# Performance work log

Measured on AMD Instinct MI355X. Metric: run time of the kernel, lower is better.

## Reference

```python
import jax, jax.numpy as jnp
import numpy as np

B, S, D, F, E, K, R, H = 4, 1024, 1024, 512, 8, 2, 64, 256
TEMP = 1.0          # step=0 -> 0.5+0.5*cos(0)=1.0, clamp(min=0.1) -> 1.0
BW, EW, ZW = 0.3, 0.1, 1e-4


def fq(t):
    """Per-tensor symmetric int8 fake-quant with straight-through estimator."""
    s = jnp.maximum(jnp.max(jnp.abs(t)) / 127.0, 1e-8)
    q = jnp.clip(jnp.round(t / s), -128, 127) * s
    return t + jax.lax.stop_gradient(q - t)


def lora_lin(h, W, A, Bm):
    # base weight is frozen (requires_grad=False) and fake-quantized
    y = h @ fq(jax.lax.stop_gradient(W)).T + (h @ Bm.T) @ A.T
    return fq(y)


def ffn(h, w1, a1, b1, w2, a2, b2, w3, a3, b3):
    # use_swiglu=True path: gate = sigmoid(w3(x)); out = w2(w1(x)*gate); dropout=eval identity
    gate = jax.nn.sigmoid(lora_lin(h, w3, a3, b3))
    out = lora_lin(lora_lin(h, w1, a1, b1) * gate, w2, a2, b2)
    return fq(out)


def setup_inputs() -> dict:
    key = jax.random.key(0)
    k = jax.random.split(key, 32)
    n = lambda i, shp: jax.random.normal(k[i], shp, dtype=jnp.float32) * 0.02
    return {
        "x": jax.random.normal(k[0], (B, S, D), dtype=jnp.float32),
        "scorer_w": n(1, (E, D)), "scorer_b": jnp.zeros((E,), jnp.float32),
        "p1_w": n(2, (H, D)), "p1_b": jnp.zeros((H,), jnp.float32),
        "p2_w": n(3, (E, H)), "p2_b": jnp.zeros((E,), jnp.float32),
        "ew1_w": n(4, (E, F, D)), "ew1_a": n(5, (E, F, R)), "ew1_b": n(6, (E, R, D)),
        "ew2_w": n(7, (E, D, F)), "ew2_a": n(8, (E, D, R)), "ew2_b": n(9, (E, R, F)),
        "ew3_w": n(10, (E, F, D)), "ew3_a": n(11, (E, F, R)), "ew3_b": n(12, (E, R, D)),
        "s1_w": n(13, (F, D)), "s1_a": n(14, (F, R)), "s1_b": n(15, (R, D)),
        "s2_w": n(16, (D, F)), "s2_a": n(17, (D, R)), "s2_b": n(18, (R, F)),
        "s3_w": n(19, (F, D)), "s3_a": n(20, (F, R)), "s3_b": n(21, (R, D)),
    }


def reference(x, scorer_w, scorer_b, p1_w, p1_b, p2_w, p2_b,
              ew1_w, ew1_a, ew1_b, ew2_w, ew2_a, ew2_b, ew3_w, ew3_a, ew3_b,
              s1_w, s1_a, s1_b, s2_w, s2_a, s2_b, s3_w, s3_a, s3_b):
    xf = x.reshape(-1, D)                                           # [T, D]
    # --- router (per-token) ---
    base = (xf @ scorer_w.T + scorer_b) / TEMP                      # [T, E]
    policy = jax.nn.softmax(jax.nn.relu(xf @ p1_w.T + p1_b) @ p2_w.T + p2_b, axis=-1)
    scores = jax.nn.softmax((base + policy) * 0.5, axis=-1)         # fp32 softmax
    entropy = -(scores * jnp.log(scores + 1e-6)).sum(-1).mean()
    z_loss = ZW * (jax.nn.logsumexp(base, axis=-1) ** 2).mean()
    weights, indices = jax.lax.top_k(scores, K)                     # [T, K]
    weights = weights * TEMP
    cw = (jax.nn.one_hot(indices, E, dtype=weights.dtype) * weights[..., None]).sum(1)  # [T, E]
    usage = cw.sum(0)                                               # [E]
    uf = usage / (usage.mean() + 1e-6)
    balance_loss = BW * jnp.var(uf, ddof=1) - EW * entropy + z_loss
    # --- expert dispatch: dense masked combine (faithful to weighted scatter-add) ---
    eout = jax.vmap(lambda w1, a1, b1, w2, a2, b2, w3, a3, b3:
                    ffn(xf, w1, a1, b1, w2, a2, b2, w3, a3, b3))(
        ew1_w, ew1_a, ew1_b, ew2_w, ew2_a, ew2_b, ew3_w, ew3_a, ew3_b)  # [E, T, D]
    y = jnp.einsum('te,etd->td', cw, eout)                          # weighted combine
    z = ffn(xf, s1_w, s1_a, s1_b, s2_w, s2_a, s2_b, s3_w, s3_a, s3_b)
    out = (y + z).reshape(x.shape)
    return (out, usage, balance_loss, jnp.float32(0.0), jnp.float32(0.0))
```

## Files before the change

kernel.cpp:

```cpp
#include <hip/hip_runtime.h>

#define TTOK 4096
#define DDIM 1024
#define FDIM 512
#define NEXP 8
#define HDIM 256
#define RLORA 64
#define CROWS 14336

using u16 = unsigned short;
using f4v = __attribute__((ext_vector_type(4))) float;
using bfrag = __attribute__((ext_vector_type(8))) short;
using u16x8 = __attribute__((ext_vector_type(8))) unsigned short;

static __device__ __forceinline__ float bf2f(u16 u) {
  union { unsigned int u; float f; } x; x.u = ((unsigned int)u) << 16; return x.f;
}
static __device__ __forceinline__ u16 f2bf(float f) {
  union { float f; unsigned int u; } x; x.f = f;
  unsigned int r = (x.u + 0x7fffu + ((x.u >> 16) & 1u)) >> 16;
  return (u16)r;
}
static __device__ __forceinline__ float fq1(float t, float s) {
  float q = rintf(t / s);
  q = fminf(fmaxf(q, -128.f), 127.f);
  return q * s;
}

struct GemmGArgs {
  const u16* A; const u16* B; u16* C;
  const int* tokmap; const int2* blkmap; const int* nbrow;
};

#define STAGE1(d, kt, h, l) \
  __builtin_amdgcn_global_load_lds( \
    (const __attribute__((address_space(1))) void*)(gs[(h)*2+(l)] + (size_t)(kt)*64), \
    (__attribute__((address_space(3))) void*)&lds[(d)*32768 + (h)*8192 + (tid + (l)*512)*8], \
    16, 0, 0)

template <int MODE>
__global__ __launch_bounds__(512, 2) void gemm256g(GemmGArgs g) {
  const int bid = blockIdx.x;
  const int logical = (bid & 7) * 28 + (bid >> 3);
  const int br = logical >> 2;
  if (br >= g.nbrow[0]) return;
  const int2 bm = g.blkmap[br];
  const int e = bm.x;
  const int m0 = bm.y;
  const int n0 = (logical & 3) * 256;
  const int tid = threadIdx.x;
  const int lane = tid & 63;
  const int wave = tid >> 6;
  const int wr = wave >> 2;
  const int wc = wave & 3;

  constexpr int K = MODE ? 1024 : 512;
  const u16* Bp = g.B + (size_t)e * (MODE ? 1048576 : 524288);

  __shared__ u16 lds[65536];

  const u16* gs[8];
#pragma unroll
  for (int h = 0; h < 4; h++)
#pragma unroll
    for (int l = 0; l < 2; l++) {
      const int slot = tid + l * 512;
      const int row = slot >> 3, p = slot & 7;
      const int glog = p ^ (row & 7);
      const u16* basep;
      if (h < 2) {
        const int grow = m0 + h * 128 + row;
        const int t = MODE ? g.tokmap[grow] : grow;
        basep = g.A + (size_t)t * K;
      } else {
        basep = Bp + (size_t)(n0 + (h - 2) * 128 + row) * K;
      }
      gs[h * 2 + l] = basep + glog * 8;
    }

  f4v acc[8][4];
#pragma unroll
  for (int i = 0; i < 8; i++)
#pragma unroll
    for (int j = 0; j < 4; j++) acc[i][j] = (f4v){0.f, 0.f, 0.f, 0.f};

  const int q = lane >> 4;
  const int lx = lane & 7;
  const int l15 = lane & 15;

#pragma unroll
  for (int h = 0; h < 4; h++) { STAGE1(0, 0, h, 0); STAGE1(0, 0, h, 1); }
  __syncthreads();

  constexpr int nt = K >> 6;
  for (int kt = 0; kt < nt; ++kt) {
    const int d = kt & 1;
    const int dn = d ^ 1;
    const bool more = (kt + 1 < nt);
#pragma unroll
    for (int kk = 0; kk < 2; ++kk) {
      if (more) {
        if (kk == 0) { STAGE1(dn, kt + 1, 0, 0); STAGE1(dn, kt + 1, 0, 1);
                       STAGE1(dn, kt + 1, 1, 0); STAGE1(dn, kt + 1, 1, 1); }
        else         { STAGE1(dn, kt + 1, 2, 0); STAGE1(dn, kt + 1, 2, 1);
                       STAGE1(dn, kt + 1, 3, 0); STAGE1(dn, kt + 1, 3, 1); }
      }
      bfrag afr[8], bfr[4];
      const int pa = ((kk * 4 + q) ^ lx) << 3;
      const int abase = d * 32768 + wr * 8192 + l15 * 64 + pa;
#pragma unroll
      for (int mi = 0; mi < 8; mi++) afr[mi] = *(const bfrag*)&lds[abase + mi * 1024];
      const int bbase = d * 32768 + (2 + (wc >> 1)) * 8192 + (((wc & 1) << 6) + l15) * 64 + pa;
#pragma unroll
      for (int ni = 0; ni < 4; ni++) bfr[ni] = *(const bfrag*)&lds[bbase + ni * 1024];
      __builtin_amdgcn_s_setprio(1);
#pragma unroll
      for (int mi = 0; mi < 8; mi++)
#pragma unroll
        for (int ni = 0; ni < 4; ni++)
          acc[mi][ni] = __builtin_amdgcn_mfma_f32_16x16x32_bf16(afr[mi], bfr[ni], acc[mi][ni], 0, 0, 0);
      __builtin_amdgcn_s_setprio(0);
    }
    __syncthreads();
  }

  const int crow0 = m0 + wr * 128 + q * 4;

  if (MODE == 1) {
    u16* stage = lds;
    const int lrow0 = wr * 128 + q * 4;
    if (wc >= 2) {
      const int lc = (wc - 2) * 64 + l15;
#pragma unroll
      for (int mi = 0; mi < 8; mi++)
#pragma unroll
        for (int ni = 0; ni < 4; ni++)
#pragma unroll
          for (int r = 0; r < 4; r++)
            stage[(lrow0 + mi * 16 + r) * 136 + lc + ni * 16] = f2bf(acc[mi][ni][r]);
    }
    __syncthreads();
    if (wc < 2) {
      const int lc = wc * 64 + l15;
      const int fbase = (n0 >> 1) + lc;
#pragma unroll
      for (int mi = 0; mi < 8; mi++)
#pragma unroll
        for (int r = 0; r < 4; r++) {
          const int rowg = crow0 + mi * 16 + r;
          const int lr = lrow0 + mi * 16 + r;
#pragma unroll
          for (int ni = 0; ni < 4; ni++) {
            float y1 = acc[mi][ni][r];
            float y3 = bf2f(stage[lr * 136 + lc + ni * 16]);
            float h = y1 / (1.f + __expf(-y3));
            g.C[(size_t)rowg * FDIM + fbase + ni * 16] = f2bf(h);
          }
        }
    }
  } else {
    const int ccol0 = n0 + wc * 64 + l15;
#pragma unroll
    for (int mi = 0; mi < 8; mi++)
#pragma unroll
      for (int ni = 0; ni < 4; ni++) {
        const int col = ccol0 + ni * 16;
#pragma unroll
        for (int r = 0; r < 4; r++)
          g.C[(size_t)(crow0 + mi * 16 + r) * 1024 + col] = f2bf(acc[mi][ni][r]);
      }
  }
}

struct MidArgs {
  const u16* A64; const u16* B64; u16* C64; const float* bias64;
  const u16* A0; const u16* B0;
  const u16* Wb;
  u16* C13; u16* C2e;
  const float* amaxP;
};

__global__ __launch_bounds__(256) void mid_kernel(MidArgs g) {
  __shared__ u16 smem[25600];
  __shared__ float s_sw;
  const int bid = blockIdx.x;
  const int tid = threadIdx.x;
  const int lane = tid & 63;
  const int wave = tid >> 6;

  if (bid < 256) {
    const int wr = wave >> 1, wc = wave & 1;
    const int m0 = (bid & 63) * 64, n0 = (bid >> 6) * 64;
    const int K = DDIM, N = HDIM;
    u16* As = smem;
    u16* Bs = smem + 2048;

    const int ldrow = tid >> 2;
    const int swzcol = (((tid & 3) ^ ((tid >> 3) & 3)) << 3);
    const u16* ga = g.A64 + (size_t)(m0 + ldrow) * K + swzcol;
    const u16* gb = g.B64 + (size_t)(n0 + ldrow) * K + swzcol;

    f4v acc[2][2];
#pragma unroll
    for (int i = 0; i < 2; i++)
#pragma unroll
      for (int j = 0; j < 2; j++) acc[i][j] = (f4v){0.f, 0.f, 0.f, 0.f};

    const int rbase = lane & 15;
    const int q = lane >> 4;
    const int pg = (q ^ ((rbase >> 1) & 3)) << 3;
    const int arow = (wr << 5) + rbase;
    const int brow = (wc << 5) + rbase;

    for (int kt = 0; kt < K; kt += 32) {
      __builtin_amdgcn_global_load_lds((const __attribute__((address_space(1))) void*)(ga),
          (__attribute__((address_space(3))) void*)&As[tid * 8], 16, 0, 0);
      __builtin_amdgcn_global_load_lds((const __attribute__((address_space(1))) void*)(gb),
          (__attribute__((address_space(3))) void*)&Bs[tid * 8], 16, 0, 0);
      ga += 32; gb += 32;
      __syncthreads();
      bfrag af[2], bf[2];
#pragma unroll
      for (int mi = 0; mi < 2; mi++)
        af[mi] = *(const bfrag*)&As[(arow + mi * 16) * 32 + pg];
#pragma unroll
      for (int ni = 0; ni < 2; ni++)
        bf[ni] = *(const bfrag*)&Bs[(brow + ni * 16) * 32 + pg];
#pragma unroll
      for (int mi = 0; mi < 2; mi++)
#pragma unroll
        for (int ni = 0; ni < 2; ni++)
          acc[mi][ni] = __builtin_amdgcn_mfma_f32_16x16x32_bf16(af[mi], bf[ni], acc[mi][ni], 0, 0, 0);
      __syncthreads();
    }

    const int crow0 = m0 + (wr << 5) + ((lane >> 4) << 2);
    const int ccol0 = n0 + (wc << 5) + (lane & 15);
#pragma unroll
    for (int mi = 0; mi < 2; mi++)
#pragma unroll
      for (int ni = 0; ni < 2; ni++) {
        const int n = ccol0 + ni * 16;
        const float b = g.bias64[n];
#pragma unroll
        for (int r = 0; r < 4; r++) {
          float v = fmaxf(acc[mi][ni][r] + b, 0.f);
          g.C64[(size_t)(crow0 + mi * 16 + r) * N + n] = f2bf(v);
        }
      }
    return;
  }

  const int fid = bid - 256;
  const int z = fid >> 6;
  const int rem = fid & 63;
  const int bx = rem & 7, by = rem >> 3;
  const bool is13 = z < 18;
  if (is13 ? (bx >= 4) : (by >= 4)) return;
  const int N = is13 ? 1024 : 512;
  const int K = 64;
  const u16* Ap = is13 ? g.A0 + (size_t)z * 32768 : g.A0 + 589824 + (size_t)(z - 18) * 65536;
  const u16* Bp = is13 ? g.B0 + (size_t)z * 65536 : g.B0 + 1179648 + (size_t)(z - 18) * 32768;
  const u16* Wf = g.Wb + (size_t)z * 524288;
  u16* Cb; int flag;
  if (is13) {
    const int slot = (z >= 16) ? 8 : (z & 7);
    Cb = g.C13 + (size_t)slot * 1048576;
    flag = (z >= 8 && z < 16) || z == 17 ? 2 : 1;
  } else {
    Cb = g.C2e + (size_t)(z - 18) * 524288;
    flag = 0;
  }

  const int wr = wave >> 1, wc = wave & 1;
  const int m0 = bx * 128, n0 = by * 128;
  u16* As = smem;
  u16* Bs = smem + 4096;
  u16* stage = smem + 8192;

  if (wave == 0) {
    float m = fmaxf(g.amaxP[z * 128 + lane], g.amaxP[z * 128 + 64 + lane]);
#pragma unroll
    for (int off = 32; off > 0; off >>= 1) m = fmaxf(m, __shfl_xor(m, off));
    if (lane == 0) s_sw = fmaxf(m / 127.f, 1e-8f);
  }

  const int ldrow = tid >> 2;
  const int swzcol = (((tid & 3) ^ ((tid >> 3) & 3)) << 3);
  const u16* ga = Ap + (size_t)(m0 + ldrow) * K + swzcol;
  const u16* gb = Bp + (size_t)(n0 + ldrow) * K + swzcol;
  const size_t rowstep = (size_t)64 * K;

  f4v acc[4][4];
#pragma unroll
  for (int i = 0; i < 4; i++)
#pragma unroll
    for (int j = 0; j < 4; j++) acc[i][j] = (f4v){0.f, 0.f, 0.f, 0.f};

  const int rbase = lane & 15;
  const int q = lane >> 4;
  const int pg = (q ^ ((rbase >> 1) & 3)) << 3;
  const int arow = (wr << 6) + rbase;
  const int brow = (wc << 6) + rbase;

  for (int kt = 0; kt < K; kt += 32) {
    __builtin_amdgcn_global_load_lds((const __attribute__((address_space(1))) void*)(ga),
        (__attribute__((address_space(3))) void*)&As[tid * 8], 16, 0, 0);
    __builtin_amdgcn_global_load_lds((const __attribute__((address_space(1))) void*)(ga + rowstep),
        (__attribute__((address_space(3))) void*)&As[(256 + tid) * 8], 16, 0, 0);
    __builtin_amdgcn_global_load_lds((const __attribute__((address_space(1))) void*)(gb),
        (__attribute__((address_space(3))) void*)&Bs[tid * 8], 16, 0, 0);
    __builtin_amdgcn_global_load_lds((const __attribute__((address_space(1))) void*)(gb + rowstep),
        (__attribute__((address_space(3))) void*)&Bs[(256 + tid) * 8], 16, 0, 0);
    ga += 32; gb += 32;
    __syncthreads();
    bfrag af[4], bf[4];
#pragma unroll
    for (int mi = 0; mi < 4; mi++)
      af[mi] = *(const bfrag*)&As[(arow + mi * 16) * 32 + pg];
#pragma unroll
    for (int ni = 0; ni < 4; ni++)
      bf[ni] = *(const bfrag*)&Bs[(brow + ni * 16) * 32 + pg];
#pragma unroll
    for (int mi = 0; mi < 4; mi++)
#pragma unroll
      for (int ni = 0; ni < 4; ni++)
        acc[mi][ni] = __builtin_amdgcn_mfma_f32_16x16x32_bf16(af[mi], bf[ni], acc[mi][ni], 0, 0, 0);
    __syncthreads();
  }

  const int lrow0 = (wr << 6) + ((lane >> 4) << 2);
  const int lcol0 = (wc << 6) + (lane & 15);
#pragma unroll
  for (int mi = 0; mi < 4; mi++)
#pragma unroll
    for (int ni = 0; ni < 4; ni++) {
      const int n = lcol0 + ni * 16;
#pragma unroll
      for (int r = 0; r < 4; r++)
        stage[(lrow0 + mi * 16 + r) * 136 + n] = f2bf(acc[mi][ni][r]);
    }
  __syncthreads();
  const float sw = s_sw;

  const int dm0 = flag ? (((m0 >> 7) << 8) + (flag == 2 ? 128 : 0)) : m0;
#pragma unroll
  for (int j = 0; j < 8; j++) {
    const int s = j * 256 + tid;
    const int lr = s >> 4;
    const int n8 = (s & 15) << 3;
    const u16x8 wv = *(const u16x8*)&Wf[(size_t)(m0 + lr) * N + n0 + n8];
    const bfrag sv = *(const bfrag*)&stage[lr * 136 + n8];
    u16x8 o;
#pragma unroll
    for (int k = 0; k < 8; k++)
      o[k] = f2bf(fq1(bf2f(wv[k]), sw) + bf2f((u16)sv[k]));
    *(u16x8*)&Cb[(size_t)(dm0 + lr) * N + n0 + n8] = o;
  }
}

struct PrepArgs {
  const float* W[27]; u16* Wraw; float* amaxP;
  const float* xf; u16* xfb;
  const float* p1w; u16* p1wb;
  const float* Asrc[27]; u16* Adst;
  const float* Bsrc[27]; u16* Bdst;
};
__global__ __launch_bounds__(256) void prep_kernel(PrepArgs a) {
  const int bid = blockIdx.x;
  const int tid = threadIdx.x;
  if (bid < 3456) {
    const int t = bid >> 7;
    const int bx = bid & 127;
    const float4* src = (const float4*)a.W[t];
    ushort4* dst = (ushort4*)(a.Wraw + (size_t)t * 524288);
    const int i0 = bx * 256 + tid;
    float4 v0 = src[i0];
    float4 v1 = src[i0 + 32768];
    float4 v2 = src[i0 + 65536];
    float4 v3 = src[i0 + 98304];
    ushort4 o0, o1, o2, o3;
    o0.x = f2bf(v0.x); o0.y = f2bf(v0.y); o0.z = f2bf(v0.z); o0.w = f2bf(v0.w);
    o1.x = f2bf(v1.x); o1.y = f2bf(v1.y); o1.z = f2bf(v1.z); o1.w = f2bf(v1.w);
    o2.x = f2bf(v2.x); o2.y = f2bf(v2.y); o2.z = f2bf(v2.z); o2.w = f2bf(v2.w);
    o3.x = f2bf(v3.x); o3.y = f2bf(v3.y); o3.z = f2bf(v3.z); o3.w = f2bf(v3.w);
    dst[i0] = o0; dst[i0 + 32768] = o1; dst[i0 + 65536] = o2; dst[i0 + 98304] = o3;
    float m01 = fmaxf(fmaxf(fabsf(v0.x), fabsf(v0.y)), fmaxf(fabsf(v0.z), fabsf(v0.w)));
    float m11 = fmaxf(fmaxf(fabsf(v1.x), fabsf(v1.y)), fmaxf(fabsf(v1.z), fabsf(v1.w)));
    float m21 = fmaxf(fmaxf(fabsf(v2.x), fabsf(v2.y)), fmaxf(fabsf(v2.z), fabsf(v2.w)));
    float m31 = fmaxf(fmaxf(fabsf(v3.x), fabsf(v3.y)), fmaxf(fabsf(v3.z), fabsf(v3.w)));
    float lmax = fmaxf(fmaxf(m01, m11), fmaxf(m21, m31));
#pragma unroll
    for (int off = 32; off > 0; off >>= 1) lmax = fmaxf(lmax, __shfl_xor(lmax, off));
    __shared__ float wm[4];
    if ((tid & 63) == 0) wm[tid >> 6] = lmax;
    __syncthreads();
    if (tid == 0)
      a.amaxP[t * 128 + bx] = fmaxf(fmaxf(wm[0], wm[1]), fmaxf(wm[2], wm[3]));
    return;
  }
  const int cid = bid - 3456;
  const int slice = cid >> 10;
  const int g0 = (cid & 1023) * 256 + tid;
  const int stride = 262144;
  if (slice == 0) {
    for (int i = g0; i < 1048576; i += stride) {
      float4 v = ((const float4*)a.xf)[i];
      ushort4 o; o.x = f2bf(v.x); o.y = f2bf(v.y); o.z = f2bf(v.z); o.w = f2bf(v.w);
      ((ushort4*)a.xfb)[i] = o;
    }
  } else if (slice == 1) {
    for (int i = g0; i < 65536; i += stride) {
      float4 v = ((const float4*)a.p1w)[i];
      ushort4 o; o.x = f2bf(v.x); o.y = f2bf(v.y); o.z = f2bf(v.z); o.w = f2bf(v.w);
      ((ushort4*)a.p1wb)[i] = o;
    }
  } else if (slice == 2) {
    for (int i = g0; i < 1179648; i += stride) {
      int t, off;
      if (i < 589824) { t = i >> 15; off = i & 32767; }
      else { int j = i - 589824; t = 18 + (j >> 16); off = j & 65535; }
      a.Adst[i] = f2bf(a.Asrc[t][off]);
    }
  } else {
    for (int i = g0; i < 1474560; i += stride) {
      int t, src;
      if (i < 1179648) { t = i >> 16; int off = i & 65535; src = (off & 63) * 1024 + (off >> 6); }
      else { int j = i - 1179648; t = 18 + (j >> 15); int off = j & 32767; src = (off & 63) * 512 + (off >> 6); }
      a.Bdst[i] = f2bf(a.Bsrc[t][src]);
    }
  }
}

struct RouterArgs {
  const float* xf; const u16* ph;
  const float* sw; const float* sb;
  const float* p2w; const float* p2b;
  int* idx2; float2* wb;
  float* partials;
  int* histArr;
};
__global__ __launch_bounds__(256) void router_kernel(RouterArgs a) {
  __shared__ float sw[8][1024];
  __shared__ float p2[8][256];
  __shared__ float blog[16][8];
  __shared__ float plog[16][8];
  __shared__ int hist[8];
  const int tid = threadIdx.x;
  {
    const float4* s0 = (const float4*)a.sw;
    float4* d0 = (float4*)&sw[0][0];
    for (int i = tid; i < 2048; i += 256) d0[i] = s0[i];
    const float4* s1 = (const float4*)a.p2w;
    float4* d1 = (float4*)&p2[0][0];
    for (int i = tid; i < 512; i += 256) d1[i] = s1[i];
  }
  if (tid < 8) hist[tid] = 0;
  __syncthreads();
  const int tl = tid >> 4, s = tid & 15;
  const int token = blockIdx.x * 16 + tl;
  {
    float acc[8] = {0,0,0,0,0,0,0,0}, pacc[8] = {0,0,0,0,0,0,0,0};
    const float4* xrow = (const float4*)(a.xf + (size_t)token * 1024);
    for (int i = 0; i < 16; i++) {
      const int d4 = i * 16 + s;
      float4 xv = xrow[d4];
#pragma unroll
      for (int e = 0; e < 8; e++) {
        float4 wv = ((const float4*)&sw[e][0])[d4];
        acc[e] += xv.x * wv.x + xv.y * wv.y + xv.z * wv.z + xv.w * wv.w;
      }
    }
    const u16* phrow = a.ph + (size_t)token * 256;
    for (int i = 0; i < 16; i++) {
      const int h = i * 16 + s;
      float pv = bf2f(phrow[h]);
#pragma unroll
      for (int e = 0; e < 8; e++) pacc[e] += pv * p2[e][h];
    }
#pragma unroll
    for (int off = 8; off > 0; off >>= 1)
#pragma unroll
      for (int e = 0; e < 8; e++) {
        acc[e] += __shfl_xor(acc[e], off);
        pacc[e] += __shfl_xor(pacc[e], off);
      }
    if (s == 0) {
#pragma unroll
      for (int e = 0; e < 8; e++) {
        blog[tl][e] = acc[e] + a.sb[e];
        plog[tl][e] = pacc[e] + a.p2b[e];
      }
    }
  }
  __syncthreads();

  float vals[10];
#pragma unroll
  for (int v = 0; v < 10; v++) vals[v] = 0.f;
  if (tid < 16) {
    const int tok = blockIdx.x * 16 + tid;
    float b[8], p[8];
#pragma unroll
    for (int e = 0; e < 8; e++) { b[e] = blog[tid][e]; p[e] = plog[tid][e]; }
    float pm = p[0];
#pragma unroll
    for (int e = 1; e < 8; e++) pm = fmaxf(pm, p[e]);
    float pe[8], psum = 0.f;
#pragma unroll
    for (int e = 0; e < 8; e++) { pe[e] = expf(p[e] - pm); psum += pe[e]; }
    const float pinv = 1.f / psum;
    float sl[8];
#pragma unroll
    for (int e = 0; e < 8; e++) sl[e] = (b[e] + pe[e] * pinv) * 0.5f;
    float sm = sl[0];
#pragma unroll
    for (int e = 1; e < 8; e++) sm = fmaxf(sm, sl[e]);
    float sc[8], ssum = 0.f;
#pragma unroll
    for (int e = 0; e < 8; e++) { sc[e] = expf(sl[e] - sm); ssum += sc[e]; }
    const float sinv = 1.f / ssum;
    float ent = 0.f;
#pragma unroll
    for (int e = 0; e < 8; e++) { float v = sc[e] * sinv; sc[e] = v; ent -= v * logf(v + 1e-6f); }
    float bm = b[0];
#pragma unroll
    for (int e = 1; e < 8; e++) bm = fmaxf(bm, b[e]);
    float zs = 0.f;
#pragma unroll
    for (int e = 0; e < 8; e++) zs += expf(b[e] - bm);
    const float lse = logf(zs) + bm;
    float m1 = -1e30f, m2 = -1e30f; int i1 = 0, i2 = 0;
#pragma unroll
    for (int e = 0; e < 8; e++) {
      float v = sc[e];
      if (v > m1) { m2 = m1; i2 = i1; m1 = v; i1 = e; }
      else if (v > m2) { m2 = v; i2 = e; }
    }
    a.idx2[tok] = i1 | (i2 << 8);
    a.wb[tok] = make_float2(m1, m2);
    atomicAdd(&hist[i1], 1);
    atomicAdd(&hist[i2], 1);
    vals[0] = ent; vals[1] = lse * lse;
    vals[2 + i1] = m1; vals[2 + i2] = m2;
  }
  if (tid < 64) {
#pragma unroll
    for (int v = 0; v < 10; v++)
#pragma unroll
      for (int off = 32; off > 0; off >>= 1) vals[v] += __shfl_down(vals[v], off);
    if (tid == 0)
#pragma unroll
      for (int v = 0; v < 10; v++) a.partials[blockIdx.x * 10 + v] = vals[v];
  }
  __syncthreads();
  if (tid < 8) a.histArr[blockIdx.x * 8 + tid] = hist[tid];
}

__global__ __launch_bounds__(256) void compact_setup(const int* idx2, const int* histArr,
                                                     int2* blkmap, int* nbrow, int* tokmap,
                                                     int* posb, const float* partials, float* tail) {
  const int e = blockIdx.x;
  const int tid = threadIdx.x;
  const int lane = tid & 63, wv = tid >> 6;
  __shared__ int scnt[8];
  __shared__ int wcnt[4][8];

  {
    int local[8];
#pragma unroll
    for (int i = 0; i < 8; i++) local[i] = histArr[tid * 8 + i];
#pragma unroll
    for (int i = 0; i < 8; i++) {
      int v = local[i];
#pragma unroll
      for (int off = 32; off > 0; off >>= 1) v += __shfl_down(v, off);
      if (lane == 0) wcnt[wv][i] = v;
    }
  }
  __syncthreads();
  if (tid < 8) scnt[tid] = wcnt[0][tid] + wcnt[1][tid] + wcnt[2][tid] + wcnt[3][tid];
  __syncthreads();

  if (e == 8) {
    __shared__ float wpart[4][10];
    float pv[10];
#pragma unroll
    for (int v = 0; v < 10; v++) pv[v] = partials[tid * 10 + v];
#pragma unroll
    for (int v = 0; v < 10; v++) {
      float t = pv[v];
#pragma unroll
      for (int off = 32; off > 0; off >>= 1) t += __shfl_down(t, off);
      if (lane == 0) wpart[wv][v] = t;
    }
    __syncthreads();
    if (tid == 0) {
      float pt[10];
#pragma unroll
      for (int v = 0; v < 10; v++)
        pt[v] = wpart[0][v] + wpart[1][v] + wpart[2][v] + wpart[3][v];
      const float ent = pt[0], z = pt[1];
      float us[8];
      for (int ex = 0; ex < 8; ex++) us[ex] = pt[2 + ex];
      float tot = 0.f;
      for (int ex = 0; ex < 8; ex++) tot += us[ex];
      const float meanu = tot / 8.f;
      float uf[8], mu = 0.f;
      for (int ex = 0; ex < 8; ex++) { uf[ex] = us[ex] / (meanu + 1e-6f); mu += uf[ex]; }
      mu /= 8.f;
      float var = 0.f;
      for (int ex = 0; ex < 8; ex++) { float d = uf[ex] - mu; var += d * d; }
      var /= 7.f;
      const float bl = 0.3f * var - 0.1f * (ent / 4096.f) + 1e-4f * (z / 4096.f);
      for (int ex = 0; ex < 8; ex++) tail[ex] = us[ex];
      tail[8] = bl; tail[9] = 0.f; tail[10] = 0.f;
      int o = 0, nb = 16;
      for (int i = 0; i < 16; i++) blkmap[i] = make_int2(8, i * 256);
      for (int ex = 0; ex < 8; ex++) {
        const int nbe = (scnt[ex] + 255) >> 8;
        for (int i = 0; i < nbe; i++) blkmap[nb++] = make_int2(ex, 4096 + o + i * 256);
        o += nbe << 8;
      }
      nbrow[0] = nb;
    }
    for (int t = tid; t < 4096; t += 256) tokmap[t] = t;
    return;
  }

  __shared__ int wtot[4];
  __shared__ int carry;
  if (tid == 0) carry = 0;
  __syncthreads();
  int off = 0;
  for (int i = 0; i < e; i++) off += ((scnt[i] + 255) >> 8) << 8;
  const int base = 4096 + off;
  for (int c = 0; c < 16; c++) {
    const int t = c * 256 + tid;
    const int ii = idx2[t];
    const int i1 = ii & 255, i2 = ii >> 8;
    const int flag = (i1 == e || i2 == e) ? 1 : 0;
    const unsigned long long m = __ballot(flag);
    const int pre = __popcll(m & ((1ull << lane) - 1ull));
    if (lane == 63) wtot[wv] = pre + flag;
    __syncthreads();
    int wbase = 0;
    for (int i = 0; i < wv; i++) wbase += wtot[i];
    if (flag) {
      const int row = base + carry + wbase + pre;
      tokmap[row] = t;
      posb[t * 2 + (i2 == e ? 1 : 0)] = row;
    }
    __syncthreads();
    if (tid == 0) carry += wtot[0] + wtot[1] + wtot[2] + wtot[3];
    __syncthreads();
  }
  const int ce = scnt[e];
  const int pend = ((ce + 255) >> 8) << 8;
  for (int r = ce + tid; r < pend; r += 256) tokmap[base + r] = 0;
}

__global__ __launch_bounds__(256) void combine_g(const u16* y2c, const int* posb,
                                                 const float2* wb, float* out) {
  const int t = blockIdx.x;
  const int c = threadIdx.x;
  const float2 w = wb[t];
  const int p1 = posb[t * 2], p2 = posb[t * 2 + 1];
  ushort4 s = ((const ushort4*)(y2c + (size_t)t * 1024))[c];
  ushort4 a = ((const ushort4*)(y2c + (size_t)p1 * 1024))[c];
  ushort4 b = ((const ushort4*)(y2c + (size_t)p2 * 1024))[c];
  float4 o;
  o.x = bf2f(s.x) + w.x * bf2f(a.x) + w.y * bf2f(b.x);
  o.y = bf2f(s.y) + w.x * bf2f(a.y) + w.y * bf2f(b.y);
  o.z = bf2f(s.z) + w.x * bf2f(a.z) + w.y * bf2f(b.z);
  o.w = bf2f(s.w) + w.x * bf2f(a.w) + w.y * bf2f(b.w);
  ((float4*)(out + (size_t)t * 1024))[c] = o;
}

extern "C" void kernel_launch(void* const* d_in, const int* in_sizes, int n_in,
                              void* d_out, int out_size, void* d_ws, size_t ws_size,
                              hipStream_t stream) {
  const float* x = (const float*)d_in[0];
  const float* scorer_w = (const float*)d_in[1];
  const float* scorer_b = (const float*)d_in[2];
  const float* p1_w = (const float*)d_in[3];
  const float* p1_b = (const float*)d_in[4];
  const float* p2_w = (const float*)d_in[5];
  const float* p2_b = (const float*)d_in[6];
  const float* ew1_w = (const float*)d_in[7];
  const float* ew1_a = (const float*)d_in[8];
  const float* ew1_b = (const float*)d_in[9];
  const float* ew2_w = (const float*)d_in[10];
  const float* ew2_a = (const float*)d_in[11];
  const float* ew2_b = (const float*)d_in[12];
  const float* ew3_w = (const float*)d_in[13];
  const float* ew3_a = (const float*)d_in[14];
  const float* ew3_b = (const float*)d_in[15];
  const float* s1_w = (const float*)d_in[16];
  const float* s1_a = (const float*)d_in[17];
  const float* s1_b = (const float*)d_in[18];
  const float* s2_w = (const float*)d_in[19];
  const float* s2_a = (const float*)d_in[20];
  const float* s2_b = (const float*)d_in[21];
  const float* s3_w = (const float*)d_in[22];
  const float* s3_a = (const float*)d_in[23];
  const float* s3_b = (const float*)d_in[24];
  float* outf = (float*)d_out;

  char* w = (char*)d_ws;
  auto alloc = [&](size_t bytes) { char* p = w; w += (bytes + 255) & ~(size_t)255; return p; };
  u16* xfb  = (u16*)alloc((size_t)TTOK * DDIM * 2);
  u16* ph   = (u16*)alloc((size_t)TTOK * HDIM * 2);
  u16* p1wb = (u16*)alloc((size_t)HDIM * DDIM * 2);
  u16* Adst = (u16*)alloc((size_t)1179648 * 2);
  u16* Bdst = (u16*)alloc((size_t)1474560 * 2);
  u16* Wraw = (u16*)alloc((size_t)27 * 524288 * 2);
  u16* W13  = (u16*)alloc((size_t)9 * 1024 * 1024 * 2);
  u16* W2e  = (u16*)alloc((size_t)9 * 1024 * 512 * 2);
  u16* h2c  = (u16*)alloc((size_t)CROWS * FDIM * 2);
  u16* y2c  = (u16*)alloc((size_t)CROWS * DDIM * 2);
  float* partials = (float*)alloc(256 * 10 * 4);
  float* amaxP = (float*)alloc(27 * 128 * 4);
  int* histArr = (int*)alloc(256 * 8 * 4);
  int2* blkmap = (int2*)alloc(64 * 8);
  int* nbrow  = (int*)alloc(4);
  int* tokmap = (int*)alloc(CROWS * 4);
  int* posb   = (int*)alloc(TTOK * 2 * 4);
  int* idx2   = (int*)alloc(TTOK * 4);
  float2* wb  = (float2*)alloc(TTOK * 8);

  {
    PrepArgs a{};
    for (int e = 0; e < 8; e++) {
      a.W[e] = ew1_w + (size_t)e * 524288;
      a.W[8 + e] = ew3_w + (size_t)e * 524288;
      a.W[18 + e] = ew2_w + (size_t)e * 524288;
      a.Asrc[e] = ew1_a + (size_t)e * 32768;
      a.Asrc[8 + e] = ew3_a + (size_t)e * 32768;
      a.Asrc[18 + e] = ew2_a + (size_t)e * 65536;
      a.Bsrc[e] = ew1_b + (size_t)e * 65536;
      a.Bsrc[8 + e] = ew3_b + (size_t)e * 65536;
      a.Bsrc[18 + e] = ew2_b + (size_t)e * 32768;
    }
    a.W[16] = s1_w; a.W[17] = s3_w; a.W[26] = s2_w;
    a.Asrc[16] = s1_a; a.Asrc[17] = s3_a; a.Asrc[26] = s2_a;
    a.Bsrc[16] = s1_b; a.Bsrc[17] = s3_b; a.Bsrc[26] = s2_b;
    a.Wraw = Wraw; a.amaxP = amaxP;
    a.xf = x; a.xfb = xfb; a.p1w = p1_w; a.p1wb = p1wb;
    a.Adst = Adst; a.Bdst = Bdst;
    hipLaunchKernelGGL(prep_kernel, dim3(7552), dim3(256), 0, stream, a);
  }
  {
    MidArgs g{};
    g.A64 = xfb; g.B64 = p1wb; g.C64 = ph; g.bias64 = p1_b;
    g.A0 = Adst; g.B0 = Bdst; g.Wb = Wraw; g.C13 = W13; g.C2e = W2e; g.amaxP = amaxP;
    hipLaunchKernelGGL(mid_kernel, dim3(1984), dim3(256), 0, stream, g);
  }
  {
    RouterArgs r{};
    r.xf = x; r.ph = ph; r.sw = scorer_w; r.sb = scorer_b;
    r.p2w = p2_w; r.p2b = p2_b;
    r.idx2 = idx2; r.wb = wb; r.partials = partials; r.histArr = histArr;
    hipLaunchKernelGGL(router_kernel, dim3(256), dim3(256), 0, stream, r);
  }
  hipLaunchKernelGGL(compact_setup, dim3(9), dim3(256), 0, stream,
                     idx2, histArr, blkmap, nbrow, tokmap, posb, partials,
                     outf + (size_t)TTOK * DDIM);
  {
    GemmGArgs g{xfb, W13, h2c, tokmap, blkmap, nbrow};
    hipLaunchKernelGGL(gemm256g<1>, dim3(224), dim3(512), 0, stream, g);
  }
  {
    GemmGArgs g{h2c, W2e, y2c, tokmap, blkmap, nbrow};
    hipLaunchKernelGGL(gemm256g<0>, dim3(224), dim3(512), 0, stream, g);
  }
  hipLaunchKernelGGL(combine_g, dim3(4096), dim3(256), 0, stream, y2c, posb, wb, outf);
}
```

Baseline: 150.3 us.

## Split GEMM main loop into half-tile phases with fine-grained vmcnt barriers

Restructures the grouped 256x256 GEMM main loop into two phases per k-tile. Each phase issues part of the next tile's async global-to-LDS loads, waits on partial vmcnt counts instead of a full __syncthreads, and computes half of the M rows with B fragments reused across both phases. This aims to overlap memory loads with MFMA more finely and cut full-barrier stalls. Launch bounds move to one block per SM, which frees registers for larger fragment arrays but may lower occupancy, and the hand-counted waitcnt values are fragile.

```diff
diff --git a/kernel.cpp b/kernel.cpp
--- a/kernel.cpp
+++ b/kernel.cpp
@@ -32,14 +32,14 @@
   const int* tokmap; const int2* blkmap; const int* nbrow;
 };
 
-#define STAGE1(d, kt, h, l) \
+#define STG(d, kt, h, l) \
   __builtin_amdgcn_global_load_lds( \
     (const __attribute__((address_space(1))) void*)(gs[(h)*2+(l)] + (size_t)(kt)*64), \
     (__attribute__((address_space(3))) void*)&lds[(d)*32768 + (h)*8192 + (tid + (l)*512)*8], \
     16, 0, 0)
 
 template <int MODE>
-__global__ __launch_bounds__(512, 2) void gemm256g(GemmGArgs g) {
+__global__ __launch_bounds__(512, 1) void gemm256g(GemmGArgs g) {
   const int bid = blockIdx.x;
   const int logical = (bid & 7) * 28 + (bid >> 3);
   const int br = logical >> 2;
@@ -87,42 +87,73 @@
   const int q = lane >> 4;
   const int lx = lane & 7;
   const int l15 = lane & 15;
-
-#pragma unroll
-  for (int h = 0; h < 4; h++) { STAGE1(0, 0, h, 0); STAGE1(0, 0, h, 1); }
-  __syncthreads();
+  const int arowbase = wr * 8192 + l15 * 64;
+  const int browbase = (2 + (wc >> 1)) * 8192 + (((wc & 1) << 6) + l15) * 64;
+
+  STG(0, 0, 2, 0); STG(0, 0, 2, 1);
+  STG(0, 0, 3, 0); STG(0, 0, 3, 1);
+  STG(0, 0, 0, 0); STG(0, 0, 1, 0);
+  STG(0, 0, 0, 1); STG(0, 0, 1, 1);
 
   constexpr int nt = K >> 6;
+  bfrag bfr[2][4];
   for (int kt = 0; kt < nt; ++kt) {
     const int d = kt & 1;
     const int dn = d ^ 1;
     const bool more = (kt + 1 < nt);
-#pragma unroll
-    for (int kk = 0; kk < 2; ++kk) {
-      if (more) {
-        if (kk == 0) { STAGE1(dn, kt + 1, 0, 0); STAGE1(dn, kt + 1, 0, 1);
-                       STAGE1(dn, kt + 1, 1, 0); STAGE1(dn, kt + 1, 1, 1); }
-        else         { STAGE1(dn, kt + 1, 2, 0); STAGE1(dn, kt + 1, 2, 1);
-                       STAGE1(dn, kt + 1, 3, 0); STAGE1(dn, kt + 1, 3, 1); }
+    const int ab = d * 32768 + arowbase;
+    const int bb = d * 32768 + browbase;
+
+    asm volatile("s_waitcnt vmcnt(2)" ::: "memory");
+    __builtin_amdgcn_s_barrier();
+    if (more) { STG(dn, kt + 1, 2, 0); STG(dn, kt + 1, 2, 1);
+                STG(dn, kt + 1, 3, 0); STG(dn, kt + 1, 3, 1); }
+    {
+      bfrag afr[4][2];
+#pragma unroll
+      for (int kk = 0; kk < 2; kk++) {
+        const int pa = ((kk * 4 + q) ^ lx) << 3;
+#pragma unroll
+        for (int mi = 0; mi < 4; mi++) afr[mi][kk] = *(const bfrag*)&lds[ab + mi * 1024 + pa];
+#pragma unroll
+        for (int ni = 0; ni < 4; ni++) bfr[kk][ni] = *(const bfrag*)&lds[bb + ni * 1024 + pa];
       }
-      bfrag afr[8], bfr[4];
-      const int pa = ((kk * 4 + q) ^ lx) << 3;
-      const int abase = d * 32768 + wr * 8192 + l15 * 64 + pa;
-#pragma unroll
-      for (int mi = 0; mi < 8; mi++) afr[mi] = *(const bfrag*)&lds[abase + mi * 1024];
-      const int bbase = d * 32768 + (2 + (wc >> 1)) * 8192 + (((wc & 1) << 6) + l15) * 64 + pa;
-#pragma unroll
-      for (int ni = 0; ni < 4; ni++) bfr[ni] = *(const bfrag*)&lds[bbase + ni * 1024];
       __builtin_amdgcn_s_setprio(1);
 #pragma unroll
-      for (int mi = 0; mi < 8; mi++)
-#pragma unroll
-        for (int ni = 0; ni < 4; ni++)
-          acc[mi][ni] = __builtin_amdgcn_mfma_f32_16x16x32_bf16(afr[mi], bfr[ni], acc[mi][ni], 0, 0, 0);
+      for (int kk = 0; kk < 2; kk++)
+#pragma unroll
+        for (int mi = 0; mi < 4; mi++)
+#pragma unroll
+          for (int ni = 0; ni < 4; ni++)
+            acc[mi][ni] = __builtin_amdgcn_mfma_f32_16x16x32_bf16(afr[mi][kk], bfr[kk][ni], acc[mi][ni], 0, 0, 0);
       __builtin_amdgcn_s_setprio(0);
     }
-    __syncthreads();
-  }
+
+    if (more) asm volatile("s_waitcnt vmcnt(4)" ::: "memory");
+    else      asm volatile("s_waitcnt vmcnt(0)" ::: "memory");
+    __builtin_amdgcn_s_barrier();
+    if (more) { STG(dn, kt + 1, 0, 0); STG(dn, kt + 1, 1, 0);
+                STG(dn, kt + 1, 0, 1); STG(dn, kt + 1, 1, 1); }
+    {
+      bfrag afr[4][2];
+#pragma unroll
+      for (int kk = 0; kk < 2; kk++) {
+        const int pa = ((kk * 4 + q) ^ lx) << 3;
+#pragma unroll
+        for (int mi = 0; mi < 4; mi++) afr[mi][kk] = *(const bfrag*)&lds[ab + (mi + 4) * 1024 + pa];
+      }
+      __builtin_amdgcn_s_setprio(1);
+#pragma unroll
+      for (int kk = 0; kk < 2; kk++)
+#pragma unroll
+        for (int mi = 0; mi < 4; mi++)
+#pragma unroll
+          for (int ni = 0; ni < 4; ni++)
+            acc[mi + 4][ni] = __builtin_amdgcn_mfma_f32_16x16x32_bf16(afr[mi][kk], bfr[kk][ni], acc[mi + 4][ni], 0, 0, 0);
+      __builtin_amdgcn_s_setprio(0);
+    }
+  }
+  __syncthreads();
 
   const int crow0 = m0 + wr * 128 + q * 4;
 
```

Result: no change. 152.3 us (+1.3%).
